# Performance work log

Measured on AMD Instinct MI355X. Metric: run time of the kernel, lower is better.

## Reference

```python
import jax, jax.numpy as jnp
import numpy as np

N_QUBITS = 14
N_LAYERS = 5
N_ACTIONS = 2
BETA = 1.0
BATCH = 2048
DIM = 2 ** N_QUBITS

# static diagonal sign tables (wire 0 = most significant bit)
_idx = np.arange(DIM)

def _bit(q):
    return (_idx >> (N_QUBITS - 1 - q)) & 1

# CZ ring: all CZ gates are diagonal and commute -> fold into one sign vector
_pairs = [(i, i + 1) for i in range(N_QUBITS - 1)] + ([(N_QUBITS - 1, 0)] if N_QUBITS > 2 else [])
_ring = np.ones(DIM, np.float32)
for _q1, _q2 in _pairs:
    _ring *= np.where((_bit(_q1) & _bit(_q2)) == 1, -1.0, 1.0).astype(np.float32)
RING_SIGN = jnp.asarray(_ring)
# Z tensor Z ... tensor Z eigenvalues: parity of bitstring
_zz = np.where(np.array([bin(i).count('1') for i in range(DIM)]) % 2 == 1, -1.0, 1.0).astype(np.float32)
ZZ_SIGN = jnp.asarray(_zz)


def _rx(t):
    c = jnp.cos(t / 2).astype(jnp.complex64)
    s = (-1j) * jnp.sin(t / 2).astype(jnp.complex64)
    return jnp.stack([jnp.stack([c, s], -1), jnp.stack([s, c], -1)], -2)


def _ry(t):
    c = jnp.cos(t / 2).astype(jnp.complex64)
    s = jnp.sin(t / 2).astype(jnp.complex64)
    return jnp.stack([jnp.stack([c, -s], -1), jnp.stack([s, c], -1)], -2)


def _rz(t):
    em = jnp.exp(-1j * t / 2).astype(jnp.complex64)
    ep = jnp.exp(1j * t / 2).astype(jnp.complex64)
    z = jnp.zeros_like(em)
    return jnp.stack([jnp.stack([em, z], -1), jnp.stack([z, ep], -1)], -2)


def _apply_1q(state, U, q):
    # state: (B, 2^n) complex64; U: (2,2) shared or (B,2,2) per-sample
    B = state.shape[0]
    s = state.reshape(B, 2 ** q, 2, 2 ** (N_QUBITS - q - 1))
    if U.ndim == 2:
        s = jnp.einsum('ij,bljr->blir', U, s)
    else:
        s = jnp.einsum('bij,bljr->blir', U, s)
    return s.reshape(B, DIM)


def _circuit(theta, inp):
    # inp: (B, N_LAYERS * N_QUBITS) encoding angles; returns (B, 1) expval of Z^n
    B = inp.shape[0]
    state = jnp.zeros((B, DIM), jnp.complex64).at[:, 0].set(1.0)
    vi = 0
    for l in range(N_LAYERS + 1):
        ang = theta[vi:vi + 3 * N_QUBITS].reshape(N_QUBITS, 3)
        vi += 3 * N_QUBITS
        for q in range(N_QUBITS):
            # Rx then Ry then Rz fused into one 2x2 unitary
            U = _rz(ang[q, 2]) @ _ry(ang[q, 1]) @ _rx(ang[q, 0])
            state = _apply_1q(state, U, q)
        if l < N_LAYERS:
            state = state * RING_SIGN  # CZ entangling ring
            enc = inp[:, l * N_QUBITS:(l + 1) * N_QUBITS]
            for q in range(N_QUBITS):
                state = _apply_1q(state, _rx(enc[:, q]), q)
    p = state.real ** 2 + state.imag ** 2
    return jnp.sum(p * ZZ_SIGN, axis=1, keepdims=True)


def setup_inputs() -> dict:
    key = jax.random.key(0)
    k1, k2 = jax.random.split(key, 2)
    x = jax.random.normal(k1, (BATCH, N_QUBITS), jnp.float32)
    theta = jax.random.uniform(k2, (3 * N_QUBITS * (N_LAYERS + 1),), jnp.float32) * np.float32(np.pi)
    lam = jnp.ones((N_QUBITS * N_LAYERS,), jnp.float32)
    # Alternating output layer init: [[1, -1, 1, ...]]
    w = jnp.asarray([[(-1.0) ** i for i in range(N_ACTIONS)]], jnp.float32)
    return {"x": x, "theta": theta, "lam": lam, "w": w}


def reference(x, theta, lam, w):
    inp = jnp.tile(x, (1, N_LAYERS)) * lam          # (B, L*n)
    vals = _circuit(theta, inp)                      # (B, 1)
    logits = (vals @ w) * BETA                       # (B, n_actions)
    return jax.nn.softmax(logits, axis=1)
```

## Files before the change

kernel.cpp:

```cpp
#include <hip/hip_runtime.h>
#include <hip/hip_fp16.h>
#include <math.h>

#define NQ        14
#define DIM       16384
#define NLAYERS   5
#define NTHREADS  512

typedef float vf2 __attribute__((ext_vector_type(2)));
struct c32 { float x, y; };

__host__ __device__ constexpr int lswz5(int i) {
    return i ^ ((i >> 5) & 31) ^ ((i >> 10) & 15);
}
__host__ __device__ constexpr unsigned sjc(int j) {
    return (((j >> 4) & (j >> 3)) ^ ((j >> 3) & (j >> 2)) ^
            ((j >> 2) & (j >> 1)) ^ ((j >> 1) & j)) & 1u;
}
__host__ __device__ constexpr unsigned pjc(int j) {
    return (((j >> 3) & (j >> 2)) ^ ((j >> 2) & (j >> 1)) ^ ((j >> 1) & j)) & 1u;
}

__device__ __forceinline__ c32 cmul(c32 a, c32 b) {
    return { a.x * b.x - a.y * b.y, a.x * b.y + a.y * b.x };
}
__device__ __forceinline__ vf2 sxor(vf2 v, unsigned m) {
    return vf2{ __uint_as_float(__float_as_uint(v.x) ^ m),
                __uint_as_float(__float_as_uint(v.y) ^ m) };
}

__device__ __forceinline__ unsigned pk16(vf2 v) {
    __half2 h = __float22half2_rn(float2{ v.x, v.y });
    return *reinterpret_cast<unsigned*>(&h);
}
__device__ __forceinline__ vf2 up16(unsigned u) {
    __half2 h = *reinterpret_cast<__half2*>(&u);
    float2 f = __half22float2(h);
    return vf2{ f.x, f.y };
}

__device__ __forceinline__ vf2 cmulv(vf2 g, vf2 z) {
    vf2 o;
    asm("v_pk_mul_f32 %0, %1, %2 op_sel:[1,1] op_sel_hi:[1,0] neg_lo:[0,1] neg_hi:[0,0]\n\t"
        "v_pk_fma_f32 %0, %1, %2, %0 op_sel:[0,0,0] op_sel_hi:[0,1,1]"
        : "=&v"(o) : "v"(g), "v"(z));
    return o;
}

__device__ __forceinline__ void bfr(vf2 r, vf2& A0, vf2& A1) {
    vf2 b0, b1;
    asm("v_pk_mul_f32 %0, %2, %3 op_sel:[0,0] op_sel_hi:[0,1]\n\t"
        "v_pk_fma_f32 %0, %2, %4, %0 op_sel:[1,0,0] op_sel_hi:[1,1,1] neg_lo:[1,0,0] neg_hi:[1,0,0]\n\t"
        "v_pk_mul_f32 %1, %2, %3 op_sel:[1,0] op_sel_hi:[1,1]\n\t"
        "v_pk_fma_f32 %1, %2, %4, %1 op_sel:[0,0,0] op_sel_hi:[0,1,1]"
        : "=&v"(b0), "=&v"(b1)
        : "v"(r), "v"(A0), "v"(A1));
    A0 = b0; A1 = b1;
}

#define APPLY32R(K, RV) { const vf2 rv_ = (RV); _Pragma("unroll") \
    for (int mm = 0; mm < 16; ++mm) { \
        const int r0 = ((mm >> (K)) << ((K) + 1)) | (mm & ((1 << (K)) - 1)); \
        bfr(rv_, a[r0], a[r0 | (1 << (K))]); } }
#define APPLY16R(K, RV) { const vf2 rv_ = (RV); _Pragma("unroll") \
    for (int mm = 0; mm < 8; ++mm) { \
        const int r0 = ((mm >> (K)) << ((K) + 1)) | (mm & ((1 << (K)) - 1)); \
        bfr(rv_, aa[r0], aa[r0 | (1 << (K))]); } }

#define AMASK(j) ((((j) & 1) ? (((j) & 16) ? M11 : M10) : (((j) & 16) ? M01 : M00)) \
                  ^ (sjc(j) << 31))
#define CMASK(v, j) ((((v)) ? (((j) & 8) ? C11 : C10) : (((j) & 8) ? C01 : C00)) \
                     ^ (((pjc(j) ^ ((j) & (v) & 1)) & 1u) << 31))

__device__ __forceinline__ void passB(char* stb, const vf2* GrL, const vf2* Tk, int base2) {
    vf2 a[32];
    #pragma unroll
    for (int j = 0; j < 32; ++j)
        a[j] = up16(*(const unsigned*)(stb + (base2 ^ (lswz5(j << 4) << 2))));
    #pragma unroll
    for (int j = 0; j < 32; ++j) a[j] = cmulv(Tk[j], a[j]);
    APPLY32R(4, GrL[5]); APPLY32R(3, GrL[6]); APPLY32R(2, GrL[7]);
    APPLY32R(1, GrL[8]); APPLY32R(0, GrL[9]);
    #pragma unroll
    for (int j = 0; j < 32; ++j)
        *(unsigned*)(stb + (base2 ^ (lswz5(j << 4) << 2))) = pk16(a[j]);
}

__device__ __forceinline__ void passAA(char* stb, const vf2* GrA, const vf2* GrB,
                                       const vf2* Ta, const vf2* Tb, int base1,
                                       unsigned M00, unsigned M01, unsigned M10, unsigned M11) {
    vf2 a[32];
    #pragma unroll
    for (int j = 0; j < 32; ++j)
        a[j] = up16(*(const unsigned*)(stb + (base1 ^ (lswz5(j << 9) << 2))));
    #pragma unroll
    for (int j = 0; j < 32; ++j) a[j] = cmulv(Ta[j], a[j]);
    APPLY32R(4, GrA[0]); APPLY32R(3, GrA[1]); APPLY32R(2, GrA[2]);
    APPLY32R(1, GrA[3]); APPLY32R(0, GrA[4]);
    #pragma unroll
    for (int j = 0; j < 32; ++j) a[j] = cmulv(Tb[j], sxor(a[j], AMASK(j)));
    APPLY32R(4, GrB[0]); APPLY32R(3, GrB[1]); APPLY32R(2, GrB[2]);
    APPLY32R(1, GrB[3]); APPLY32R(0, GrB[4]);
    #pragma unroll
    for (int j = 0; j < 32; ++j)
        *(unsigned*)(stb + (base1 ^ (lswz5(j << 9) << 2))) = pk16(a[j]);
}

__device__ __forceinline__ void passCC(char* stb, const vf2* GrA, const vf2* GrB,
                                       const vf2* Ta, const vf2* Tb, int base3,
                                       unsigned C00, unsigned C01, unsigned C10, unsigned C11) {
    #pragma unroll
    for (int v = 0; v < 2; ++v) {
        const int bb = base3 ^ (lswz5(v << 13) << 2);
        vf2 aa[16];
        #pragma unroll
        for (int j = 0; j < 16; ++j)
            aa[j] = up16(*(const unsigned*)(stb + (bb ^ (j << 2))));
        #pragma unroll
        for (int j = 0; j < 16; ++j) aa[j] = cmulv(Ta[j], aa[j]);
        APPLY16R(3, GrA[10]); APPLY16R(2, GrA[11]); APPLY16R(1, GrA[12]); APPLY16R(0, GrA[13]);
        #pragma unroll
        for (int j = 0; j < 16; ++j) aa[j] = cmulv(Tb[j], sxor(aa[j], CMASK(v, j)));
        APPLY16R(3, GrB[10]); APPLY16R(2, GrB[11]); APPLY16R(1, GrB[12]); APPLY16R(0, GrB[13]);
        #pragma unroll
        for (int j = 0; j < 16; ++j)
            *(unsigned*)(stb + (bb ^ (j << 2))) = pk16(aa[j]);
    }
}

__device__ __forceinline__ void passCLast(char* stb, const vf2* GrL, const vf2* Tk,
                                          int base3, float& se, float& so) {
    #pragma unroll
    for (int v = 0; v < 2; ++v) {
        const int bb = base3 ^ (lswz5(v << 13) << 2);
        vf2 aa[16];
        #pragma unroll
        for (int j = 0; j < 16; ++j)
            aa[j] = up16(*(const unsigned*)(stb + (bb ^ (j << 2))));
        #pragma unroll
        for (int j = 0; j < 16; ++j) aa[j] = cmulv(Tk[j], aa[j]);
        APPLY16R(3, GrL[10]); APPLY16R(2, GrL[11]); APPLY16R(1, GrL[12]); APPLY16R(0, GrL[13]);
        #pragma unroll
        for (int j = 0; j < 16; ++j) {
            const float d = fmaf(aa[j].x, aa[j].x, aa[j].y * aa[j].y);
            if (((v ^ __popc(j)) & 1) == 0) se += d; else so += d;
        }
    }
}

__attribute__((amdgpu_flat_work_group_size(NTHREADS, NTHREADS),
               amdgpu_waves_per_eu(4, 4)))
__global__ void pqc_kernel(
    const float* __restrict__ x,
    const float* __restrict__ theta,
    const float* __restrict__ lam,
    const float* __restrict__ w,
    float* __restrict__ out)
{
    __shared__ unsigned sth[DIM];
    __shared__ vf2 Gr[NLAYERS + 1][NQ];
    __shared__ vf2 Gang[NLAYERS + 1][NQ];
    __shared__ vf2 G0c[NQ][2];
    __shared__ vf2 F0[5][2];
    __shared__ vf2 T[15][32];
    __shared__ float wsum[NTHREADS / 64];

    const int t = threadIdx.x;
    const int b = blockIdx.x;
    char* stb = (char*)sth;

    if (t < (NLAYERS + 1) * NQ) {
        const int l = t / NQ, q = t % NQ;
        const float a0 = theta[3 * t + 0];
        const float a1 = theta[3 * t + 1];
        const float a2t = theta[3 * t + 2];
        const float cx = cosf(0.5f * a0), sx = sinf(0.5f * a0);
        const float cy = cosf(0.5f * a1), sy = sinf(0.5f * a1);
        const float cz = cosf(0.5f * a2t), sz = sinf(0.5f * a2t);
        const c32 m00 = {  cy * cx,  sy * sx };
        const c32 m01 = { -sy * cx, -cy * sx };
        const c32 m10 = {  sy * cx, -cy * sx };
        c32 u00 = { cz * m00.x + sz * m00.y,  cz * m00.y - sz * m00.x };
        c32 u01 = { cz * m01.x + sz * m01.y,  cz * m01.y - sz * m01.x };
        c32 u10 = { cz * m10.x - sz * m10.y,  cz * m10.y + sz * m10.x };
        if (l >= 1) {
            const float ang = x[b * NQ + q] * lam[(l - 1) * NQ + q];
            const float c = cosf(0.5f * ang), s = sinf(0.5f * ang);
            const c32 u11 = { u00.x, -u00.y };
            const c32 v00 = { u00.x * c + s * u01.y,  u00.y * c - s * u01.x };
            const c32 v10 = { u10.x * c + s * u11.y,  u10.y * c - s * u11.x };
            u00 = v00; u10 = v10;
        }
        if (l == 0) {
            G0c[q][0] = vf2{ u00.x, u00.y };
            G0c[q][1] = vf2{ u10.x, u10.y };
        }
        const float cb = sqrtf(u00.x * u00.x + u00.y * u00.y);
        const float sb = sqrtf(u10.x * u10.x + u10.y * u10.y);
        const float inv = rsqrtf(fmaxf(cb * cb + sb * sb, 1e-30f));
        const float p  = atan2f(u00.y, u00.x);
        const float qq = atan2f(u10.y, u10.x);
        Gr[l][q]   = vf2{ cb * inv, sb * inv };
        Gang[l][q] = vf2{ 0.5f * (qq - p), -0.5f * (p + qq) };
    }
    __syncthreads();

    if (t < 448) {
        const int k = 1 + (t >> 5), j = t & 31;
        const int r = k % 6;
        const int win = (r == 0 || r == 5) ? 0 : ((r == 1 || r == 4) ? 1 : 2);
        if (win != 2 || j < 16) {
            const int lc = 1 + k / 3;
            const int lp = (k >= 3) ? lc - 1 : 0;
            const int nb = (win == 2) ? 4 : 5;
            float th = 0.f;
            for (int m = 0; m < nb; ++m) {
                const int q = (win == 0) ? (4 - m) : (win == 1) ? (9 - m) : (13 - m);
                float ww = Gang[lc][q].y;
                if (lp) ww += Gang[lp][q].x;
                th += ((j >> m) & 1) ? ww : -ww;
            }
            float sn, cn;
            __sincosf(th, &sn, &cn);
            T[k][j] = vf2{ cn, sn };
        }
    } else if (t < 458) {
        const int u = t - 448, q = u >> 1, be = u & 1;
        const float c2 = Gang[1][q].y;
        const float ph = be ? c2 : -c2;
        float sn, cn;
        __sincosf(ph, &sn, &cn);
        const vf2 g = G0c[q][be];
        const c32 f = cmul(c32{ g.x, g.y }, c32{ cn, sn });
        F0[q][be] = vf2{ f.x, f.y };
    }
    __syncthreads();

    const int base1 = lswz5(t) << 2;
    const int base2 = lswz5(((t & 0x1F0) << 5) | (t & 15)) << 2;
    const int base3 = lswz5(t << 4) << 2;
    const unsigned Pp  = (unsigned)(__popc(t & (t >> 1) & 0xFF) & 1);
    const unsigned t8 = (t >> 8) & 1u, tb0 = t & 1u;
    const unsigned M00 =  Pp              << 31;
    const unsigned M10 = (Pp ^ t8)        << 31;
    const unsigned M01 = (Pp ^ tb0)       << 31;
    const unsigned M11 = (Pp ^ t8 ^ tb0)  << 31;
    const unsigned C00 =  Pp              << 31;
    const unsigned C01 = (Pp ^ tb0)       << 31;
    const unsigned C10 = (Pp ^ t8)        << 31;
    const unsigned C11 = (Pp ^ t8 ^ tb0)  << 31;

    {
        c32 pref = { G0c[5][(t >> 8) & 1].x, G0c[5][(t >> 8) & 1].y };
        #pragma unroll
        for (int qq = 6; qq <= 13; ++qq) {
            const vf2 g = G0c[qq][(t >> (13 - qq)) & 1];
            pref = cmul(pref, c32{ g.x, g.y });
        }
        c32 p01p[4], p234[8];
        #pragma unroll
        for (int k = 0; k < 4; ++k) {
            const vf2 ga = F0[0][k >> 1], gb = F0[1][k & 1];
            p01p[k] = cmul(pref, cmul(c32{ ga.x, ga.y }, c32{ gb.x, gb.y }));
        }
        #pragma unroll
        for (int m = 0; m < 8; ++m) {
            const vf2 g2 = F0[2][m >> 2], g3 = F0[3][(m >> 1) & 1], g4 = F0[4][m & 1];
            p234[m] = cmul(cmul(c32{ g2.x, g2.y }, c32{ g3.x, g3.y }), c32{ g4.x, g4.y });
        }
        vf2 a[32];
        #pragma unroll
        for (int j = 0; j < 32; ++j) {
            const c32 av = cmul(p01p[j >> 3], p234[j & 7]);
            a[j] = sxor(vf2{ av.x, av.y }, AMASK(j));
        }
        APPLY32R(4, Gr[1][0]); APPLY32R(3, Gr[1][1]); APPLY32R(2, Gr[1][2]);
        APPLY32R(1, Gr[1][3]); APPLY32R(0, Gr[1][4]);
        #pragma unroll
        for (int j = 0; j < 32; ++j)
            *(unsigned*)(stb + (base1 ^ (lswz5(j << 9) << 2))) = pk16(a[j]);
    }
    __syncthreads();

    passB(stb, Gr[1], T[1], base2);                                        __syncthreads();
    passCC(stb, Gr[1], Gr[2], T[2], T[3], base3, C00, C01, C10, C11);      __syncthreads();
    passB(stb, Gr[2], T[4], base2);                                        __syncthreads();
    passAA(stb, Gr[2], Gr[3], T[5], T[6], base1, M00, M01, M10, M11);      __syncthreads();
    passB(stb, Gr[3], T[7], base2);                                        __syncthreads();
    passCC(stb, Gr[3], Gr[4], T[8], T[9], base3, C00, C01, C10, C11);      __syncthreads();
    passB(stb, Gr[4], T[10], base2);                                       __syncthreads();
    passAA(stb, Gr[4], Gr[5], T[11], T[12], base1, M00, M01, M10, M11);    __syncthreads();
    passB(stb, Gr[5], T[13], base2);                                       __syncthreads();
    float se = 0.f, so = 0.f;
    passCLast(stb, Gr[5], T[14], base3, se, so);

    float local = (__popc(t) & 1) ? (so - se) : (se - so);
    #pragma unroll
    for (int off = 32; off > 0; off >>= 1)
        local += __shfl_down(local, off, 64);
    if ((t & 63) == 0) wsum[t >> 6] = local;
    __syncthreads();
    if (t == 0) {
        float v = 0.0f;
        #pragma unroll
        for (int i = 0; i < NTHREADS / 64; ++i) v += wsum[i];
        const float BETA = 1.0f;
        const float l0 = v * w[0] * BETA, l1 = v * w[1] * BETA;
        const float m  = fmaxf(l0, l1);
        const float e0 = __expf(l0 - m), e1 = __expf(l1 - m);
        const float inv = 1.0f / (e0 + e1);
        out[2 * b + 0] = e0 * inv;
        out[2 * b + 1] = e1 * inv;
    }
}

extern "C" void kernel_launch(void* const* d_in, const int* in_sizes, int n_in,
                              void* d_out, int out_size, void* d_ws, size_t ws_size,
                              hipStream_t stream) {
    const float* x     = (const float*)d_in[0];
    const float* theta = (const float*)d_in[1];
    const float* lam   = (const float*)d_in[2];
    const float* w     = (const float*)d_in[3];
    float* out = (float*)d_out;
    const int batch = in_sizes[0] / NQ;
    pqc_kernel<<<batch, NTHREADS, 0, stream>>>(x, theta, lam, w, out);
}
```

Before: 263.0 us.

## Restructure qubit passes into 4-qubit windows with 16-element register tiles

Replaces the 5/5/4-qubit window decomposition, which held 32 complex amplitudes per thread, with 4/4/4/2-qubit windows that process 16 amplitudes per thread in two non-unrolled halves. The phase tables shrink to 16- and 4-entry forms, and the pass schedule grows from 10 to 15 barrier-separated shared-memory passes. The aim is lower register pressure, which may allow better scheduling or fewer spills at the fixed occupancy. The cost is more fp16 round-trips through LDS and more __syncthreads calls.

```diff
diff --git a/kernel.cpp b/kernel.cpp
--- a/kernel.cpp
+++ b/kernel.cpp
@@ -13,13 +13,12 @@
 __host__ __device__ constexpr int lswz5(int i) {
     return i ^ ((i >> 5) & 31) ^ ((i >> 10) & 15);
 }
-__host__ __device__ constexpr unsigned sjc(int j) {
-    return (((j >> 4) & (j >> 3)) ^ ((j >> 3) & (j >> 2)) ^
-            ((j >> 2) & (j >> 1)) ^ ((j >> 1) & j)) & 1u;
-}
 __host__ __device__ constexpr unsigned pjc(int j) {
     return (((j >> 3) & (j >> 2)) ^ ((j >> 2) & (j >> 1)) ^ ((j >> 1) & j)) & 1u;
 }
+__host__ __device__ constexpr int OFSJ(int sh, int j) { return lswz5(j << sh) << 2; }
+#define WOFS_A (((1 << 9) | (1 << 4)) << 2)
+#define WOFS_T (((1 << 13) | (1 << 3)) << 2)
 
 __device__ __forceinline__ c32 cmul(c32 a, c32 b) {
     return { a.x * b.x - a.y * b.y, a.x * b.y + a.y * b.x };
@@ -28,7 +27,6 @@
     return vf2{ __uint_as_float(__float_as_uint(v.x) ^ m),
                 __uint_as_float(__float_as_uint(v.y) ^ m) };
 }
-
 __device__ __forceinline__ unsigned pk16(vf2 v) {
     __half2 h = __float22half2_rn(float2{ v.x, v.y });
     return *reinterpret_cast<unsigned*>(&h);
@@ -38,7 +36,6 @@
     float2 f = __half22float2(h);
     return vf2{ f.x, f.y };
 }
-
 __device__ __forceinline__ vf2 cmulv(vf2 g, vf2 z) {
     vf2 o;
     asm("v_pk_mul_f32 %0, %1, %2 op_sel:[1,1] op_sel_hi:[1,0] neg_lo:[0,1] neg_hi:[0,0]\n\t"
@@ -46,7 +43,6 @@
         : "=&v"(o) : "v"(g), "v"(z));
     return o;
 }
-
 __device__ __forceinline__ void bfr(vf2 r, vf2& A0, vf2& A1) {
     vf2 b0, b1;
     asm("v_pk_mul_f32 %0, %2, %3 op_sel:[0,0] op_sel_hi:[0,1]\n\t"
@@ -58,92 +54,100 @@
     A0 = b0; A1 = b1;
 }
 
-#define APPLY32R(K, RV) { const vf2 rv_ = (RV); _Pragma("unroll") \
-    for (int mm = 0; mm < 16; ++mm) { \
-        const int r0 = ((mm >> (K)) << ((K) + 1)) | (mm & ((1 << (K)) - 1)); \
-        bfr(rv_, a[r0], a[r0 | (1 << (K))]); } }
 #define APPLY16R(K, RV) { const vf2 rv_ = (RV); _Pragma("unroll") \
     for (int mm = 0; mm < 8; ++mm) { \
         const int r0 = ((mm >> (K)) << ((K) + 1)) | (mm & ((1 << (K)) - 1)); \
         bfr(rv_, aa[r0], aa[r0 | (1 << (K))]); } }
 
-#define AMASK(j) ((((j) & 1) ? (((j) & 16) ? M11 : M10) : (((j) & 16) ? M01 : M00)) \
-                  ^ (sjc(j) << 31))
-#define CMASK(v, j) ((((v)) ? (((j) & 8) ? C11 : C10) : (((j) & 8) ? C01 : C00)) \
-                     ^ (((pjc(j) ^ ((j) & (v) & 1)) & 1u) << 31))
-
-__device__ __forceinline__ void passB(char* stb, const vf2* GrL, const vf2* Tk, int base2) {
-    vf2 a[32];
-    #pragma unroll
-    for (int j = 0; j < 32; ++j)
-        a[j] = up16(*(const unsigned*)(stb + (base2 ^ (lswz5(j << 4) << 2))));
-    #pragma unroll
-    for (int j = 0; j < 32; ++j) a[j] = cmulv(Tk[j], a[j]);
-    APPLY32R(4, GrL[5]); APPLY32R(3, GrL[6]); APPLY32R(2, GrL[7]);
-    APPLY32R(1, GrL[8]); APPLY32R(0, GrL[9]);
-    #pragma unroll
-    for (int j = 0; j < 32; ++j)
-        *(unsigned*)(stb + (base2 ^ (lswz5(j << 4) << 2))) = pk16(a[j]);
-}
-
-__device__ __forceinline__ void passAA(char* stb, const vf2* GrA, const vf2* GrB,
-                                       const vf2* Ta, const vf2* Tb, int base1,
-                                       unsigned M00, unsigned M01, unsigned M10, unsigned M11) {
-    vf2 a[32];
-    #pragma unroll
-    for (int j = 0; j < 32; ++j)
-        a[j] = up16(*(const unsigned*)(stb + (base1 ^ (lswz5(j << 9) << 2))));
-    #pragma unroll
-    for (int j = 0; j < 32; ++j) a[j] = cmulv(Ta[j], a[j]);
-    APPLY32R(4, GrA[0]); APPLY32R(3, GrA[1]); APPLY32R(2, GrA[2]);
-    APPLY32R(1, GrA[3]); APPLY32R(0, GrA[4]);
-    #pragma unroll
-    for (int j = 0; j < 32; ++j) a[j] = cmulv(Tb[j], sxor(a[j], AMASK(j)));
-    APPLY32R(4, GrB[0]); APPLY32R(3, GrB[1]); APPLY32R(2, GrB[2]);
-    APPLY32R(1, GrB[3]); APPLY32R(0, GrB[4]);
-    #pragma unroll
-    for (int j = 0; j < 32; ++j)
-        *(unsigned*)(stb + (base1 ^ (lswz5(j << 9) << 2))) = pk16(a[j]);
-}
-
-__device__ __forceinline__ void passCC(char* stb, const vf2* GrA, const vf2* GrB,
-                                       const vf2* Ta, const vf2* Tb, int base3,
-                                       unsigned C00, unsigned C01, unsigned C10, unsigned C11) {
-    #pragma unroll
-    for (int v = 0; v < 2; ++v) {
-        const int bb = base3 ^ (lswz5(v << 13) << 2);
+#define SMW(j) ((((j) & 1) ? (((j) & 8) ? s11 : s01) : (((j) & 8) ? s10 : s00)) \
+                ^ (pjc(j) << 31))
+#define SMASK_SETUP(w) \
+    const unsigned s00 = (Pt ^ ((unsigned)(w) & t8)) << 31; \
+    const unsigned s01 = s00 ^ ((unsigned)(w) << 31); \
+    const unsigned s10 = s00 ^ (t0 << 31); \
+    const unsigned s11 = s01 ^ (t0 << 31);
+
+template<int SH>
+__device__ __forceinline__ void pass4(char* stb, const vf2* g4, const vf2* Tk,
+                                      int base) {
+    #pragma unroll 1
+    for (int w = 0; w < 2; ++w) {
+        const int bb = base ^ (w ? WOFS_T : 0);
         vf2 aa[16];
         #pragma unroll
         for (int j = 0; j < 16; ++j)
-            aa[j] = up16(*(const unsigned*)(stb + (bb ^ (j << 2))));
+            aa[j] = up16(*(const unsigned*)(stb + (bb ^ OFSJ(SH, j))));
+        #pragma unroll
+        for (int j = 0; j < 16; ++j) aa[j] = cmulv(Tk[j], aa[j]);
+        APPLY16R(3, g4[0]); APPLY16R(2, g4[1]); APPLY16R(1, g4[2]); APPLY16R(0, g4[3]);
+        #pragma unroll
+        for (int j = 0; j < 16; ++j)
+            *(unsigned*)(stb + (bb ^ OFSJ(SH, j))) = pk16(aa[j]);
+    }
+}
+
+__device__ __forceinline__ void passAA(char* stb, const vf2* gA, const vf2* gB,
+                                       const vf2* Ta, const vf2* Tb, int base,
+                                       unsigned Pt, unsigned t8, unsigned t0) {
+    #pragma unroll 1
+    for (int w = 0; w < 2; ++w) {
+        const int bb = base ^ (w ? WOFS_A : 0);
+        SMASK_SETUP(w);
+        vf2 aa[16];
+        #pragma unroll
+        for (int j = 0; j < 16; ++j)
+            aa[j] = up16(*(const unsigned*)(stb + (bb ^ OFSJ(10, j))));
         #pragma unroll
         for (int j = 0; j < 16; ++j) aa[j] = cmulv(Ta[j], aa[j]);
-        APPLY16R(3, GrA[10]); APPLY16R(2, GrA[11]); APPLY16R(1, GrA[12]); APPLY16R(0, GrA[13]);
-        #pragma unroll
-        for (int j = 0; j < 16; ++j) aa[j] = cmulv(Tb[j], sxor(aa[j], CMASK(v, j)));
-        APPLY16R(3, GrB[10]); APPLY16R(2, GrB[11]); APPLY16R(1, GrB[12]); APPLY16R(0, GrB[13]);
-        #pragma unroll
-        for (int j = 0; j < 16; ++j)
-            *(unsigned*)(stb + (bb ^ (j << 2))) = pk16(aa[j]);
-    }
-}
-
-__device__ __forceinline__ void passCLast(char* stb, const vf2* GrL, const vf2* Tk,
-                                          int base3, float& se, float& so) {
-    #pragma unroll
-    for (int v = 0; v < 2; ++v) {
-        const int bb = base3 ^ (lswz5(v << 13) << 2);
+        APPLY16R(3, gA[0]); APPLY16R(2, gA[1]); APPLY16R(1, gA[2]); APPLY16R(0, gA[3]);
+        #pragma unroll
+        for (int j = 0; j < 16; ++j) aa[j] = cmulv(Tb[j], sxor(aa[j], SMW(j)));
+        APPLY16R(3, gB[0]); APPLY16R(2, gB[1]); APPLY16R(1, gB[2]); APPLY16R(0, gB[3]);
+        #pragma unroll
+        for (int j = 0; j < 16; ++j)
+            *(unsigned*)(stb + (bb ^ OFSJ(10, j))) = pk16(aa[j]);
+    }
+}
+
+__device__ __forceinline__ void passDD(char* stb, const vf2* gA, const vf2* gB,
+                                       const vf2* Ta4, const vf2* Tb4, int base,
+                                       unsigned Pt, unsigned t8, unsigned t0) {
+    #pragma unroll 1
+    for (int w = 0; w < 2; ++w) {
+        const int bb = base ^ (w ? WOFS_T : 0);
+        SMASK_SETUP(w);
         vf2 aa[16];
         #pragma unroll
         for (int j = 0; j < 16; ++j)
-            aa[j] = up16(*(const unsigned*)(stb + (bb ^ (j << 2))));
-        #pragma unroll
-        for (int j = 0; j < 16; ++j) aa[j] = cmulv(Tk[j], aa[j]);
-        APPLY16R(3, GrL[10]); APPLY16R(2, GrL[11]); APPLY16R(1, GrL[12]); APPLY16R(0, GrL[13]);
+            aa[j] = up16(*(const unsigned*)(stb + (bb ^ OFSJ(0, j))));
+        #pragma unroll
+        for (int j = 0; j < 16; ++j) aa[j] = cmulv(Ta4[j & 3], aa[j]);
+        APPLY16R(1, gA[0]); APPLY16R(0, gA[1]);
+        #pragma unroll
+        for (int j = 0; j < 16; ++j) aa[j] = cmulv(Tb4[j & 3], sxor(aa[j], SMW(j)));
+        APPLY16R(1, gB[0]); APPLY16R(0, gB[1]);
+        #pragma unroll
+        for (int j = 0; j < 16; ++j)
+            *(unsigned*)(stb + (bb ^ OFSJ(0, j))) = pk16(aa[j]);
+    }
+}
+
+__device__ __forceinline__ void passD5(char* stb, const vf2* g, const vf2* T4e,
+                                       int base, float& se, float& so) {
+    #pragma unroll 1
+    for (int w = 0; w < 2; ++w) {
+        const int bb = base ^ (w ? WOFS_T : 0);
+        vf2 aa[16];
+        #pragma unroll
+        for (int j = 0; j < 16; ++j)
+            aa[j] = up16(*(const unsigned*)(stb + (bb ^ OFSJ(0, j))));
+        #pragma unroll
+        for (int j = 0; j < 16; ++j) aa[j] = cmulv(T4e[j & 3], aa[j]);
+        APPLY16R(1, g[0]); APPLY16R(0, g[1]);
         #pragma unroll
         for (int j = 0; j < 16; ++j) {
             const float d = fmaf(aa[j].x, aa[j].x, aa[j].y * aa[j].y);
-            if (((v ^ __popc(j)) & 1) == 0) se += d; else so += d;
+            if (((w ^ __popc(j)) & 1) == 0) se += d; else so += d;
         }
     }
 }
@@ -161,8 +165,9 @@
     __shared__ vf2 Gr[NLAYERS + 1][NQ];
     __shared__ vf2 Gang[NLAYERS + 1][NQ];
     __shared__ vf2 G0c[NQ][2];
-    __shared__ vf2 F0[5][2];
-    __shared__ vf2 T[15][32];
+    __shared__ vf2 F0[4][2];
+    __shared__ vf2 T16[14][16];
+    __shared__ vf2 T4[5][4];
     __shared__ float wsum[NTHREADS / 64];
 
     const int t = threadIdx.x;
@@ -205,94 +210,103 @@
     }
     __syncthreads();
 
-    if (t < 448) {
-        const int k = 1 + (t >> 5), j = t & 31;
-        const int r = k % 6;
-        const int win = (r == 0 || r == 5) ? 0 : ((r == 1 || r == 4) ? 1 : 2);
-        if (win != 2 || j < 16) {
-            const int lc = 1 + k / 3;
-            const int lp = (k >= 3) ? lc - 1 : 0;
-            const int nb = (win == 2) ? 4 : 5;
-            float th = 0.f;
-            for (int m = 0; m < nb; ++m) {
-                const int q = (win == 0) ? (4 - m) : (win == 1) ? (9 - m) : (13 - m);
-                float ww = Gang[lc][q].y;
-                if (lp) ww += Gang[lp][q].x;
-                th += ((j >> m) & 1) ? ww : -ww;
-            }
-            float sn, cn;
-            __sincosf(th, &sn, &cn);
-            T[k][j] = vf2{ cn, sn };
-        }
-    } else if (t < 458) {
-        const int u = t - 448, q = u >> 1, be = u & 1;
+    if (t < 224) {
+        const int id = t >> 4, j = t & 15;
+        int lp, lc, qb;
+        if (id < 5)       { lp = id;     lc = id + 1; qb = 7;  }
+        else if (id < 10) { lp = id - 5; lc = id - 4; qb = 11; }
+        else              { lp = id - 9; lc = id - 8; qb = 3;  }
+        float th = 0.f;
+        for (int m = 0; m < 4; ++m) {
+            const int q = qb - m;
+            float ww = Gang[lc][q].y;
+            if (lp) ww += Gang[lp][q].x;
+            th += ((j >> m) & 1) ? ww : -ww;
+        }
+        float sn, cn; __sincosf(th, &sn, &cn);
+        T16[id][j] = vf2{ cn, sn };
+    } else if (t < 244) {
+        const int u = t - 224, id = u >> 2, j = u & 3;
+        const int lp = id, lc = id + 1;
+        float th = 0.f;
+        for (int m = 0; m < 2; ++m) {
+            const int q = 13 - m;
+            float ww = Gang[lc][q].y;
+            if (lp) ww += Gang[lp][q].x;
+            th += ((j >> m) & 1) ? ww : -ww;
+        }
+        float sn, cn; __sincosf(th, &sn, &cn);
+        T4[id][j] = vf2{ cn, sn };
+    } else if (t < 252) {
+        const int u = t - 244, q = u >> 1, be = u & 1;
         const float c2 = Gang[1][q].y;
         const float ph = be ? c2 : -c2;
-        float sn, cn;
-        __sincosf(ph, &sn, &cn);
+        float sn, cn; __sincosf(ph, &sn, &cn);
         const vf2 g = G0c[q][be];
         const c32 f = cmul(c32{ g.x, g.y }, c32{ cn, sn });
         F0[q][be] = vf2{ f.x, f.y };
     }
     __syncthreads();
 
-    const int base1 = lswz5(t) << 2;
-    const int base2 = lswz5(((t & 0x1F0) << 5) | (t & 15)) << 2;
-    const int base3 = lswz5(t << 4) << 2;
-    const unsigned Pp  = (unsigned)(__popc(t & (t >> 1) & 0xFF) & 1);
-    const unsigned t8 = (t >> 8) & 1u, tb0 = t & 1u;
-    const unsigned M00 =  Pp              << 31;
-    const unsigned M10 = (Pp ^ t8)        << 31;
-    const unsigned M01 = (Pp ^ tb0)       << 31;
-    const unsigned M11 = (Pp ^ t8 ^ tb0)  << 31;
-    const unsigned C00 =  Pp              << 31;
-    const unsigned C01 = (Pp ^ tb0)       << 31;
-    const unsigned C10 = (Pp ^ t8)        << 31;
-    const unsigned C11 = (Pp ^ t8 ^ tb0)  << 31;
+    const int baseA = lswz5(t) << 2;
+    const int baseB = lswz5(((t >> 6) << 10) | (t & 63)) << 2;
+    const int baseC = lswz5(((t >> 2) << 6) | (t & 3)) << 2;
+    const int baseD = lswz5(t << 4) << 2;
+    const unsigned Pt = (unsigned)(__popc(t & (t >> 1) & 0xFF) & 1);
+    const unsigned t8 = (t >> 8) & 1u, t0 = t & 1u;
 
     {
         c32 pref = { G0c[5][(t >> 8) & 1].x, G0c[5][(t >> 8) & 1].y };
         #pragma unroll
-        for (int qq = 6; qq <= 13; ++qq) {
-            const vf2 g = G0c[qq][(t >> (13 - qq)) & 1];
+        for (int q = 6; q <= 13; ++q) {
+            const vf2 g = G0c[q][(t >> (13 - q)) & 1];
             pref = cmul(pref, c32{ g.x, g.y });
         }
-        c32 p01p[4], p234[8];
-        #pragma unroll
-        for (int k = 0; k < 4; ++k) {
-            const vf2 ga = F0[0][k >> 1], gb = F0[1][k & 1];
-            p01p[k] = cmul(pref, cmul(c32{ ga.x, ga.y }, c32{ gb.x, gb.y }));
-        }
-        #pragma unroll
-        for (int m = 0; m < 8; ++m) {
-            const vf2 g2 = F0[2][m >> 2], g3 = F0[3][(m >> 1) & 1], g4 = F0[4][m & 1];
-            p234[m] = cmul(cmul(c32{ g2.x, g2.y }, c32{ g3.x, g3.y }), c32{ g4.x, g4.y });
-        }
-        vf2 a[32];
-        #pragma unroll
-        for (int j = 0; j < 32; ++j) {
-            const c32 av = cmul(p01p[j >> 3], p234[j & 7]);
-            a[j] = sxor(vf2{ av.x, av.y }, AMASK(j));
-        }
-        APPLY32R(4, Gr[1][0]); APPLY32R(3, Gr[1][1]); APPLY32R(2, Gr[1][2]);
-        APPLY32R(1, Gr[1][3]); APPLY32R(0, Gr[1][4]);
-        #pragma unroll
-        for (int j = 0; j < 32; ++j)
-            *(unsigned*)(stb + (base1 ^ (lswz5(j << 9) << 2))) = pk16(a[j]);
+        #pragma unroll 1
+        for (int w2 = 0; w2 < 2; ++w2) {
+            const vf2 g4w = G0c[4][w2];
+            const c32 prefw = cmul(pref, c32{ g4w.x, g4w.y });
+            c32 pf01[4], pf23[4];
+            #pragma unroll
+            for (int k = 0; k < 4; ++k) {
+                const vf2 fa = F0[0][(k >> 1) & 1], fb = F0[1][k & 1];
+                const vf2 fc = F0[2][(k >> 1) & 1], fd = F0[3][k & 1];
+                pf01[k] = cmul(prefw, cmul(c32{ fa.x, fa.y }, c32{ fb.x, fb.y }));
+                pf23[k] = cmul(c32{ fc.x, fc.y }, c32{ fd.x, fd.y });
+            }
+            SMASK_SETUP(w2);
+            vf2 aa[16];
+            #pragma unroll
+            for (int j = 0; j < 16; ++j) {
+                const c32 av = cmul(pf01[(j >> 2) & 3], pf23[j & 3]);
+                aa[j] = sxor(vf2{ av.x, av.y }, SMW(j));
+            }
+            APPLY16R(3, Gr[1][0]); APPLY16R(2, Gr[1][1]);
+            APPLY16R(1, Gr[1][2]); APPLY16R(0, Gr[1][3]);
+            const int bb = baseA ^ (w2 ? WOFS_A : 0);
+            #pragma unroll
+            for (int j = 0; j < 16; ++j)
+                *(unsigned*)(stb + (bb ^ OFSJ(10, j))) = pk16(aa[j]);
+        }
     }
     __syncthreads();
 
-    passB(stb, Gr[1], T[1], base2);                                        __syncthreads();
-    passCC(stb, Gr[1], Gr[2], T[2], T[3], base3, C00, C01, C10, C11);      __syncthreads();
-    passB(stb, Gr[2], T[4], base2);                                        __syncthreads();
-    passAA(stb, Gr[2], Gr[3], T[5], T[6], base1, M00, M01, M10, M11);      __syncthreads();
-    passB(stb, Gr[3], T[7], base2);                                        __syncthreads();
-    passCC(stb, Gr[3], Gr[4], T[8], T[9], base3, C00, C01, C10, C11);      __syncthreads();
-    passB(stb, Gr[4], T[10], base2);                                       __syncthreads();
-    passAA(stb, Gr[4], Gr[5], T[11], T[12], base1, M00, M01, M10, M11);    __syncthreads();
-    passB(stb, Gr[5], T[13], base2);                                       __syncthreads();
+    pass4<6>(stb, &Gr[1][4], T16[0], baseB);                            __syncthreads();
+    pass4<2>(stb, &Gr[1][8], T16[5], baseC);                            __syncthreads();
+    passDD(stb, &Gr[1][12], &Gr[2][12], T4[0], T4[1], baseD, Pt, t8, t0); __syncthreads();
+    pass4<2>(stb, &Gr[2][8], T16[6], baseC);                            __syncthreads();
+    pass4<6>(stb, &Gr[2][4], T16[1], baseB);                            __syncthreads();
+    passAA(stb, &Gr[2][0], &Gr[3][0], T16[10], T16[11], baseA, Pt, t8, t0); __syncthreads();
+    pass4<6>(stb, &Gr[3][4], T16[2], baseB);                            __syncthreads();
+    pass4<2>(stb, &Gr[3][8], T16[7], baseC);                            __syncthreads();
+    passDD(stb, &Gr[3][12], &Gr[4][12], T4[2], T4[3], baseD, Pt, t8, t0); __syncthreads();
+    pass4<2>(stb, &Gr[4][8], T16[8], baseC);                            __syncthreads();
+    pass4<6>(stb, &Gr[4][4], T16[3], baseB);                            __syncthreads();
+    passAA(stb, &Gr[4][0], &Gr[5][0], T16[12], T16[13], baseA, Pt, t8, t0); __syncthreads();
+    pass4<6>(stb, &Gr[5][4], T16[4], baseB);                            __syncthreads();
+    pass4<2>(stb, &Gr[5][8], T16[9], baseC);                            __syncthreads();
     float se = 0.f, so = 0.f;
-    passCLast(stb, Gr[5], T[14], base3, se, so);
+    passD5(stb, &Gr[5][12], T4[4], baseD, se, so);
 
     float local = (__popc(t) & 1) ? (so - se) : (se - so);
     #pragma unroll
```

Measured after the change: 293.4 us. +11.6%, slower.
